# Optimization experiments

Measured on AMD Instinct MI355X. Metric: run time of the kernel, lower is better.

Reference implementation:

```python
import jax, jax.numpy as jnp
import numpy as np

CLIP_LEN = 16
IN_CH = 64  # math.ceil(256 // 4 / 4) * 4
BN_EPS = 1e-5


def setup_inputs() -> dict:
    key = jax.random.key(0)
    ks = jax.random.split(key, 7)
    x = jax.random.normal(ks[0], (128, 256, 56, 56), jnp.float32)
    bn_gamma = 1.0 + 0.1 * jax.random.normal(ks[1], (IN_CH,), jnp.float32)
    bn_beta = 0.1 * jax.random.normal(ks[2], (IN_CH,), jnp.float32)
    bn_mean = 0.1 * jax.random.normal(ks[3], (IN_CH,), jnp.float32)
    bn_var = jax.random.uniform(ks[4], (IN_CH,), jnp.float32, minval=0.5, maxval=1.5)
    # groups=2 Conv3d: out=2, in_per_group=IN_CH//2, kernel 3x3x3
    conv_w = 0.02 * jax.random.normal(ks[5], (2, IN_CH // 2, 3, 3, 3), jnp.float32)
    conv_b = 0.02 * jax.random.normal(ks[6], (2,), jnp.float32)
    return dict(x=x, bn_gamma=bn_gamma, bn_beta=bn_beta, bn_mean=bn_mean,
                bn_var=bn_var, conv_w=conv_w, conv_b=conv_b)


def _gsm(x5, bn_gamma, bn_beta, bn_mean, bn_var, conv_w, conv_b):
    # x5: [n, c, t, h, w] with c == IN_CH
    n, c, t, h, w = x5.shape
    scale = bn_gamma * jax.lax.rsqrt(bn_var + BN_EPS)          # [c]
    shift = bn_beta - bn_mean * scale                          # [c]
    x_act = jax.nn.relu(x5 * scale[None, :, None, None, None]
                        + shift[None, :, None, None, None])
    gate = jnp.tanh(
        jax.lax.conv_general_dilated(
            x_act, conv_w, window_strides=(1, 1, 1), padding='SAME',
            dimension_numbers=('NCDHW', 'OIDHW', 'NCDHW'),
            feature_group_count=2)
        + conv_b[None, :, None, None, None])                   # [n,2,t,h,w]
    half = c // 2

    def gated_shift(xg, g, left):
        y = g * xg                                             # gated part
        r = xg - y                                             # residual part
        if left:
            y_sh = jnp.concatenate([y[:, :, 1:], jnp.zeros_like(y[:, :, :1])], axis=2)
        else:
            y_sh = jnp.concatenate([jnp.zeros_like(y[:, :, :1]), y[:, :, :-1]], axis=2)
        out = y_sh + r
        # channel regroup: [n,2,c/4,t,h,w] -> permute -> [n,c/2,t,h,w]
        return out.reshape(n, 2, half // 2, t, h, w).transpose(0, 2, 1, 3, 4, 5).reshape(n, half, t, h, w)

    y1 = gated_shift(x5[:, :half], gate[:, 0:1], left=True)
    y2 = gated_shift(x5[:, half:], gate[:, 1:2], left=False)
    return jnp.concatenate([y1, y2], axis=1)


def reference(x, bn_gamma, bn_beta, bn_mean, bn_var, conv_w, conv_b):
    nt, c, h, w = x.shape
    n = nt // CLIP_LEN
    # [nt, IN_CH, h, w] -> [n, IN_CH, T, h, w]
    xs = x[:, :IN_CH].reshape(n, CLIP_LEN, IN_CH, h, w).transpose(0, 2, 1, 3, 4)
    y = _gsm(xs, bn_gamma, bn_beta, bn_mean, bn_var, conv_w, conv_b)
    y = y.transpose(0, 2, 1, 3, 4).reshape(nt, IN_CH, h, w)
    # remaining channels pass through unchanged; net wrapper is identity
    return jnp.concatenate([y, x[:, IN_CH:]], axis=1)
```

## Files before the change

kernel.cpp:

```cpp
#include <hip/hip_runtime.h>
#include <hip/hip_cooperative_groups.h>
#include <math.h>

namespace cg = cooperative_groups;

namespace {
constexpr int kT = 16;
constexpr int kH = 56;
constexpr int kW = 56;
constexpr int kCAll = 256;
constexpr int kPlane = kH * kW;
constexpr int kPlane4 = kPlane / 4;
constexpr size_t kGateBytes = (size_t)256 * kPlane * sizeof(float);
constexpr int kSpan = 192 * kPlane4;
constexpr int kFrame4 = kCAll * kPlane4;
}


__device__ __forceinline__ void conv_block(
    int bid, int tid, const float* __restrict__ x,
    const float* __restrict__ gamma, const float* __restrict__ beta,
    const float* __restrict__ mean, const float* __restrict__ var,
    const float* __restrict__ cw, const float* __restrict__ cb,
    float* __restrict__ gate, float4* smb) {
  const int stripe = bid & 1;
  const int g = (bid >> 1) & 1;
  const int t = (bid >> 2) & 15;
  const int n = bid >> 6;
  const int h0 = stripe * 28;
  const int wid = tid >> 6;
  const int lane = tid & 63;
  const int r = lane >> 1;
  const int h = lane & 1;
  const int wbase = wid * 510;

  for (int i = lane; i < 510; i += 64)
    smb[wbase + i] = make_float4(0.f, 0.f, 0.f, 0.f);

  int rr_u[7], fb_u[7], go_u[7];
  bool val_u[7];
  #pragma unroll
  for (int u = 0; u < 7; ++u) {
    const int j = lane + u * 64;
    bool v = (j < 420);
    int rr = 0, fb = 0, go = 0;
    if (v) {
      rr = j / 14;
      fb = j - rr * 14;
      const int gr = h0 + rr - 1;
      v = ((unsigned)gr < (unsigned)kH);
      if (v) go = gr * 14 + fb;
    }
    rr_u[u] = rr; fb_u[u] = fb; go_u[u] = go; val_u[u] = v;
  }

  float acc[28];
  #pragma unroll
  for (int p = 0; p < 28; ++p) acc[p] = 0.f;

  auto loadS = [&](int s, float4 (&pf)[7]) {
    const int il = s / 3;
    const int kd = s - il * 3;
    const int tt = t + kd - 1;
    const int ch = g * 32 + wid * 8 + il;
    if (tt >= 0 && tt < kT) {
      const float4* src4 =
          (const float4*)x + ((size_t)(n * kT + tt) * kCAll + ch) * kPlane4;
      #pragma unroll
      for (int u = 0; u < 7; ++u)
        pf[u] = val_u[u] ? src4[go_u[u]] : make_float4(0.f, 0.f, 0.f, 0.f);
    } else {
      #pragma unroll
      for (int u = 0; u < 7; ++u) pf[u] = make_float4(0.f, 0.f, 0.f, 0.f);
    }
  };

  auto stageS = [&](int s, const float4 (&pf)[7]) {
    const int il = s / 3;
    const int kd = s - il * 3;
    const int tt = t + kd - 1;
    if (tt < 0 || tt >= kT) return;
    const int ch = g * 32 + wid * 8 + il;
    const float sc = gamma[ch] * rsqrtf(var[ch] + 1e-5f);
    const float sh = beta[ch] - mean[ch] * sc;
    #pragma unroll
    for (int u = 0; u < 7; ++u) {
      if (val_u[u]) {
        float4 a = pf[u];
        a.x = fmaxf(0.f, fmaf(a.x, sc, sh));
        a.y = fmaxf(0.f, fmaf(a.y, sc, sh));
        a.z = fmaxf(0.f, fmaf(a.z, sc, sh));
        a.w = fmaxf(0.f, fmaf(a.w, sc, sh));
        smb[wbase + rr_u[u] * 17 + fb_u[u] + 1] = a;
      }
    }
  };

  auto computeS = [&](int s) {
    const int il = s / 3;
    const int kd = s - il * 3;
    const int tt = t + kd - 1;
    if (tt < 0 || tt >= kT) return;
    if (r >= 28) return;
    const int ch = g * 32 + wid * 8 + il;
    const float* wbp = cw + ch * 27 + kd * 9;
    float wk[9];
    #pragma unroll
    for (int j = 0; j < 9; ++j) wk[j] = wbp[j];
    #pragma unroll
    for (int kh = 0; kh < 3; ++kh) {
      const int base = wbase + (r + kh) * 17 + 7 * h;
      float f[36];
      #pragma unroll
      for (int jj = 0; jj < 9; ++jj) {
        const float4 B = smb[base + jj];
        f[4 * jj + 0] = B.x; f[4 * jj + 1] = B.y;
        f[4 * jj + 2] = B.z; f[4 * jj + 3] = B.w;
      }
      const float w0 = wk[kh * 3 + 0];
      const float w1 = wk[kh * 3 + 1];
      const float w2 = wk[kh * 3 + 2];
      #pragma unroll
      for (int p = 0; p < 28; ++p)
        acc[p] = fmaf(f[p + 3], w0,
                 fmaf(f[p + 4], w1, fmaf(f[p + 5], w2, acc[p])));
    }
  };

  float4 A[7], B[7];
  loadS(0, A);
  for (int s2 = 0; s2 < 24; s2 += 2) {
    if (s2 + 1 < 24) loadS(s2 + 1, B);
    stageS(s2, A);
    computeS(s2);
    if (s2 + 2 < 24) loadS(s2 + 2, A);
    if (s2 + 1 < 24) { stageS(s2 + 1, B); computeS(s2 + 1); }
  }

  __syncthreads();
  float* smf = (float*)smb;
  if (r < 28) {
    const int q0 = r * 56 + h * 28;
    #pragma unroll
    for (int p = 0; p < 28; ++p) smf[wid * 1568 + q0 + p] = acc[p];
  }
  __syncthreads();
  const float bias = cb[g];
  float* gp = gate + ((size_t)(n * 2 + g) * kT + t) * kPlane + h0 * kW;
  for (int q = tid; q < 1568; q += 256) {
    float s = smf[q] + smf[1568 + q] + smf[2 * 1568 + q] + smf[3 * 1568 + q];
    gp[q] = tanhf(s + bias);
  }
}

__device__ __forceinline__ void copy_engine(
    int engine, int nengines, int tid, const float4* __restrict__ x4,
    float4* __restrict__ o4, int nf, int skip_hole) {
  const size_t stride = (size_t)nengines * 256;
  const size_t total = (size_t)nf * kSpan;
  size_t j = (size_t)engine * 256 + tid;
  auto mapidx = [&](size_t jj, size_t& idx, bool& ok) {
    const int f = (int)(jj / kSpan);
    const int within = (int)(jj - (size_t)f * kSpan);
    ok = !(skip_hole && f == 126 && within < 3 * kPlane4);
    idx = (size_t)f * kFrame4 + 64 * kPlane4 + within;
  };
  for (; j + 3 * stride < total; j += 4 * stride) {
    size_t i0, i1, i2, i3; bool k0, k1, k2, k3;
    mapidx(j, i0, k0); mapidx(j + stride, i1, k1);
    mapidx(j + 2 * stride, i2, k2); mapidx(j + 3 * stride, i3, k3);
    const float4 a = x4[i0], b = x4[i1], c = x4[i2], d = x4[i3];
    if (k0) o4[i0] = a;
    if (k1) o4[i1] = b;
    if (k2) o4[i2] = c;
    if (k3) o4[i3] = d;
  }
  for (; j < total; j += stride) {
    size_t i0; bool k0;
    mapidx(j, i0, k0);
    const float4 a = x4[i0];
    if (k0) o4[i0] = a;
  }
}

__device__ __forceinline__ void shift_columns(
    int q0, int qstride, const float4* __restrict__ x4,
    const float4* __restrict__ g4, float4* __restrict__ o4) {
  const size_t xstep = (size_t)kFrame4;
  for (int q = q0; q < 8 * 2 * 32 * kPlane4; q += qstride) {
    const int p = q % kPlane4;
    const int rem = q / kPlane4;
    const int m = rem & 31;
    const int half = (rem >> 5) & 1;
    const int n = rem >> 6;
    const int src_ch = half * 32 + m;
    const int k = 2 * (m & 15) + (m >> 4);
    const int c = half * 32 + k;
    const float4* xp = x4 + ((size_t)(n * kT) * kCAll + src_ch) * kPlane4 + p;
    const float4* gp = g4 + (size_t)((n * 2 + half) * kT) * kPlane4 + p;
    float4* op = o4 + ((size_t)(n * kT) * kCAll + c) * kPlane4 + p;
    if (half == 0) {
      float4 xc = xp[0], gc = gp[0];
      #pragma unroll
      for (int t = 0; t < kT; ++t) {
        float4 xn = make_float4(0.f, 0.f, 0.f, 0.f);
        float4 gn = make_float4(0.f, 0.f, 0.f, 0.f);
        if (t < kT - 1) { xn = xp[(size_t)(t + 1) * xstep]; gn = gp[(t + 1) * kPlane4]; }
        float4 res;
        res.x = gn.x * xn.x + xc.x - gc.x * xc.x;
        res.y = gn.y * xn.y + xc.y - gc.y * xc.y;
        res.z = gn.z * xn.z + xc.z - gc.z * xc.z;
        res.w = gn.w * xn.w + xc.w - gc.w * xc.w;
        op[(size_t)t * xstep] = res;
        xc = xn; gc = gn;
      }
    } else {
      float4 xprev = make_float4(0.f, 0.f, 0.f, 0.f);
      float4 gprev = make_float4(0.f, 0.f, 0.f, 0.f);
      #pragma unroll
      for (int t = 0; t < kT; ++t) {
        const float4 xc = xp[(size_t)t * xstep];
        const float4 gc = gp[t * kPlane4];
        float4 res;
        res.x = gprev.x * xprev.x + xc.x - gc.x * xc.x;
        res.y = gprev.y * xprev.y + xc.y - gc.y * xc.y;
        res.z = gprev.z * xprev.z + xc.z - gc.z * xc.z;
        res.w = gprev.w * xprev.w + xc.w - gc.w * xc.w;
        op[(size_t)t * xstep] = res;
        xprev = xc; gprev = gc;
      }
    }
  }
}

__global__ __launch_bounds__(256, 4)
void coop_fused_kernel(const float* __restrict__ x,
                       const float* __restrict__ gamma,
                       const float* __restrict__ beta,
                       const float* __restrict__ mean,
                       const float* __restrict__ var,
                       const float* __restrict__ cw,
                       const float* __restrict__ cb,
                       float* __restrict__ gate,
                       const float4* __restrict__ x4,
                       float4* __restrict__ o4) {
  __shared__ float4 smb[4 * 510];
  if (blockIdx.x & 1)
    conv_block(blockIdx.x >> 1, threadIdx.x, x, gamma, beta, mean, var, cw, cb,
               gate, smb);
  else
    copy_engine(blockIdx.x >> 1, 512, threadIdx.x, x4, o4, 128, 0);
  cg::this_grid().sync();
  shift_columns(blockIdx.x * 256 + threadIdx.x, 1024 * 256, x4,
                (const float4*)gate, o4);
}

__global__ __launch_bounds__(256, 2)
void fused_conv_copy_kernel(const float* __restrict__ x,
                            const float* __restrict__ gamma,
                            const float* __restrict__ beta,
                            const float* __restrict__ mean,
                            const float* __restrict__ var,
                            const float* __restrict__ cw,
                            const float* __restrict__ cb,
                            float* __restrict__ gate,
                            const float4* __restrict__ x4,
                            float4* __restrict__ o4,
                            int nf_copy, int skip_hole) {
  __shared__ float4 smb[4 * 510];
  if ((blockIdx.x & 1) == 0) {
    copy_engine(blockIdx.x >> 1, 512, threadIdx.x, x4, o4, nf_copy, skip_hole);
    return;
  }
  conv_block(blockIdx.x >> 1, threadIdx.x, x, gamma, beta, mean, var, cw, cb,
             gate, smb);
}

__global__ __launch_bounds__(256)
void copy_gate_slice_kernel(float4* __restrict__ o4) {
  const int j = blockIdx.x * 256 + threadIdx.x;
  if (j >= 3 * kPlane4) return;
  const int q = j / kPlane4;
  const int rr = j - q * kPlane4;
  const int pidx = (q == 0) ? 239 : (q == 1 ? 254 : 255);
  const size_t G1 = (size_t)127 * kCAll * kPlane4;
  const size_t H = ((size_t)126 * kCAll + 64) * kPlane4;
  o4[H + j] = o4[G1 + (size_t)pidx * kPlane4 + rr];
}

__global__ __launch_bounds__(256)
void shift_c64_kernel(const float4* __restrict__ x4,
                      const float4* __restrict__ g4,
                      float4* __restrict__ o4, int nf) {
  const size_t total = (size_t)nf * 64 * kPlane4;
  const size_t j = (size_t)blockIdx.x * 256 + threadIdx.x;
  if (j >= total) return;
  const int p = (int)(j % kPlane4);
  const size_t rest = j / kPlane4;
  const int c = (int)(rest % 64);
  const int f = (int)(rest / 64);
  const int n = f >> 4;
  const int t = f & 15;
  const int half = c >> 5;
  const int k = c & 31;
  const int m = ((k & 1) << 4) + (k >> 1);
  const int src_ch = half * 32 + m;
  const size_t xcur = ((size_t)f * kCAll + src_ch) * kPlane4 + p;
  const size_t gbase = (size_t)(n * 2 + half) * kT * kPlane4 + p;
  const float4 xc = x4[xcur];
  const float4 gc = g4[gbase + (size_t)t * kPlane4];
  float4 y = make_float4(0.f, 0.f, 0.f, 0.f);
  if (half == 0) {
    if (t < kT - 1) {
      const float4 xn = x4[xcur + (size_t)kCAll * kPlane4];
      const float4 gn = g4[gbase + (size_t)(t + 1) * kPlane4];
      y.x = gn.x * xn.x; y.y = gn.y * xn.y; y.z = gn.z * xn.z; y.w = gn.w * xn.w;
    }
  } else {
    if (t > 0) {
      const float4 xp = x4[xcur - (size_t)kCAll * kPlane4];
      const float4 gp = g4[gbase + (size_t)(t - 1) * kPlane4];
      y.x = gp.x * xp.x; y.y = gp.y * xp.y; y.z = gp.z * xp.z; y.w = gp.w * xp.w;
    }
  }
  const size_t oidx = ((size_t)f * kCAll + c) * kPlane4 + p;
  float4 res;
  res.x = y.x + (xc.x - gc.x * xc.x);
  res.y = y.y + (xc.y - gc.y * xc.y);
  res.z = y.z + (xc.z - gc.z * xc.z);
  res.w = y.w + (xc.w - gc.w * xc.w);
  o4[oidx] = res;
}

__global__ __launch_bounds__(256)
void last_frame_kernel(const float4* __restrict__ x4, float4* o4) {
  const int idx = blockIdx.x * 256 + threadIdx.x;
  if (idx >= kCAll * kPlane4) return;
  const size_t F127 = (size_t)127 * kCAll * kPlane4;
  const int p = idx % kPlane4;
  const int c = idx / kPlane4;
  if (c >= 64) { o4[F127 + idx] = x4[F127 + idx]; return; }
  const size_t H = ((size_t)126 * kCAll + 64) * kPlane4;
  const int half = c >> 5;
  const int k = c & 31;
  const int m = ((k & 1) << 4) + (k >> 1);
  const int src_ch = half * 32 + m;
  const float4 xc = x4[F127 + (size_t)src_ch * kPlane4 + p];
  float4 gc;
  float4 y = make_float4(0.f, 0.f, 0.f, 0.f);
  if (half == 0) {
    gc = o4[H + 0 * kPlane4 + p];
  } else {
    gc = o4[H + 2 * kPlane4 + p];
    const float4 gp = o4[H + 1 * kPlane4 + p];
    const float4 xp = x4[((size_t)126 * kCAll + src_ch) * kPlane4 + p];
    y.x = gp.x * xp.x; y.y = gp.y * xp.y; y.z = gp.z * xp.z; y.w = gp.w * xp.w;
  }
  float4 res;
  res.x = y.x + (xc.x - gc.x * xc.x);
  res.y = y.y + (xc.y - gc.y * xc.y);
  res.z = y.z + (xc.z - gc.z * xc.z);
  res.w = y.w + (xc.w - gc.w * xc.w);
  o4[F127 + idx] = res;
}

__global__ __launch_bounds__(256)
void fix_hole_kernel(const float4* __restrict__ x4, float4* __restrict__ o4) {
  const int j = blockIdx.x * 256 + threadIdx.x;
  if (j >= 3 * kPlane4) return;
  const size_t H = ((size_t)126 * kCAll + 64) * kPlane4;
  o4[H + j] = x4[H + j];
}

extern "C" void kernel_launch(void* const* d_in, const int* in_sizes, int n_in,
                              void* d_out, int out_size, void* d_ws, size_t ws_size,
                              hipStream_t stream) {
  const float* x     = (const float*)d_in[0];
  const float* gamma = (const float*)d_in[1];
  const float* beta  = (const float*)d_in[2];
  const float* mean  = (const float*)d_in[3];
  const float* var   = (const float*)d_in[4];
  const float* cw    = (const float*)d_in[5];
  const float* cb    = (const float*)d_in[6];
  float* out = (float*)d_out;
  const float4* x4v = (const float4*)x;
  float4* o4v = (float4*)out;

  const bool have_ws = (d_ws != nullptr) && (ws_size >= kGateBytes);

  if (have_ws) {
    int maxBlocks = 0;
    hipError_t qe = hipOccupancyMaxActiveBlocksPerMultiprocessor(
        &maxBlocks, (const void*)coop_fused_kernel, 256, 0);
    if (qe == hipSuccess && maxBlocks >= 4) {
      float* gate = (float*)d_ws;
      void* args[] = {(void*)&x, (void*)&gamma, (void*)&beta, (void*)&mean,
                      (void*)&var, (void*)&cw, (void*)&cb, (void*)&gate,
                      (void*)&x4v, (void*)&o4v};
      hipError_t le = hipLaunchCooperativeKernel(
          (const void*)coop_fused_kernel, dim3(1024), dim3(256), args, 0, stream);
      if (le == hipSuccess) return;
    }
  }

  float* gate = have_ws ? (float*)d_ws : out + (size_t)127 * kCAll * kPlane;
  const int nf = have_ws ? 128 : 127;
  const int skip_hole = have_ws ? 0 : 1;

  fused_conv_copy_kernel<<<1024, 256, 0, stream>>>(
      x, gamma, beta, mean, var, cw, cb, gate, x4v, o4v, nf, skip_hole);

  if (!have_ws)
    copy_gate_slice_kernel<<<10, 256, 0, stream>>>(o4v);

  const int shift_total = nf * 64 * kPlane4;
  shift_c64_kernel<<<(shift_total + 255) / 256, 256, 0, stream>>>(
      x4v, (const float4*)gate, o4v, nf);

  if (!have_ws) {
    last_frame_kernel<<<(kCAll * kPlane4 + 255) / 256, 256, 0, stream>>>(x4v, o4v);
    fix_hole_kernel<<<10, 256, 0, stream>>>(x4v, o4v);
  }
}
```

Baseline: 216.5 us.

## Replace cooperative grid-sync kernel with two ordinary launches for conv/copy and shift

Removes the cooperative kernel that ran conv+copy, then a grid-wide sync, then the shift phase. Instead a normal conv/copy kernel is launched, followed by a separate one-thread-per-column shift kernel (1568 blocks, each thread walking the 16 frames). This drops the grid barrier and the occupancy cap (launch_bounds 256,4 with a fixed 1024-block grid), and gives the shift phase more parallel threads. It adds one extra kernel launch and relies on stream ordering for the dependency.

```diff
diff --git a/kernel.cpp b/kernel.cpp
--- a/kernel.cpp
+++ b/kernel.cpp
@@ -1,8 +1,5 @@
 #include <hip/hip_runtime.h>
-#include <hip/hip_cooperative_groups.h>
 #include <math.h>
-
-namespace cg = cooperative_groups;
 
 namespace {
 constexpr int kT = 16;
@@ -183,78 +180,6 @@
   }
 }
 
-__device__ __forceinline__ void shift_columns(
-    int q0, int qstride, const float4* __restrict__ x4,
-    const float4* __restrict__ g4, float4* __restrict__ o4) {
-  const size_t xstep = (size_t)kFrame4;
-  for (int q = q0; q < 8 * 2 * 32 * kPlane4; q += qstride) {
-    const int p = q % kPlane4;
-    const int rem = q / kPlane4;
-    const int m = rem & 31;
-    const int half = (rem >> 5) & 1;
-    const int n = rem >> 6;
-    const int src_ch = half * 32 + m;
-    const int k = 2 * (m & 15) + (m >> 4);
-    const int c = half * 32 + k;
-    const float4* xp = x4 + ((size_t)(n * kT) * kCAll + src_ch) * kPlane4 + p;
-    const float4* gp = g4 + (size_t)((n * 2 + half) * kT) * kPlane4 + p;
-    float4* op = o4 + ((size_t)(n * kT) * kCAll + c) * kPlane4 + p;
-    if (half == 0) {
-      float4 xc = xp[0], gc = gp[0];
-      #pragma unroll
-      for (int t = 0; t < kT; ++t) {
-        float4 xn = make_float4(0.f, 0.f, 0.f, 0.f);
-        float4 gn = make_float4(0.f, 0.f, 0.f, 0.f);
-        if (t < kT - 1) { xn = xp[(size_t)(t + 1) * xstep]; gn = gp[(t + 1) * kPlane4]; }
-        float4 res;
-        res.x = gn.x * xn.x + xc.x - gc.x * xc.x;
-        res.y = gn.y * xn.y + xc.y - gc.y * xc.y;
-        res.z = gn.z * xn.z + xc.z - gc.z * xc.z;
-        res.w = gn.w * xn.w + xc.w - gc.w * xc.w;
-        op[(size_t)t * xstep] = res;
-        xc = xn; gc = gn;
-      }
-    } else {
-      float4 xprev = make_float4(0.f, 0.f, 0.f, 0.f);
-      float4 gprev = make_float4(0.f, 0.f, 0.f, 0.f);
-      #pragma unroll
-      for (int t = 0; t < kT; ++t) {
-        const float4 xc = xp[(size_t)t * xstep];
-        const float4 gc = gp[t * kPlane4];
-        float4 res;
-        res.x = gprev.x * xprev.x + xc.x - gc.x * xc.x;
-        res.y = gprev.y * xprev.y + xc.y - gc.y * xc.y;
-        res.z = gprev.z * xprev.z + xc.z - gc.z * xc.z;
-        res.w = gprev.w * xprev.w + xc.w - gc.w * xc.w;
-        op[(size_t)t * xstep] = res;
-        xprev = xc; gprev = gc;
-      }
-    }
-  }
-}
-
-__global__ __launch_bounds__(256, 4)
-void coop_fused_kernel(const float* __restrict__ x,
-                       const float* __restrict__ gamma,
-                       const float* __restrict__ beta,
-                       const float* __restrict__ mean,
-                       const float* __restrict__ var,
-                       const float* __restrict__ cw,
-                       const float* __restrict__ cb,
-                       float* __restrict__ gate,
-                       const float4* __restrict__ x4,
-                       float4* __restrict__ o4) {
-  __shared__ float4 smb[4 * 510];
-  if (blockIdx.x & 1)
-    conv_block(blockIdx.x >> 1, threadIdx.x, x, gamma, beta, mean, var, cw, cb,
-               gate, smb);
-  else
-    copy_engine(blockIdx.x >> 1, 512, threadIdx.x, x4, o4, 128, 0);
-  cg::this_grid().sync();
-  shift_columns(blockIdx.x * 256 + threadIdx.x, 1024 * 256, x4,
-                (const float4*)gate, o4);
-}
-
 __global__ __launch_bounds__(256, 2)
 void fused_conv_copy_kernel(const float* __restrict__ x,
                             const float* __restrict__ gamma,
@@ -274,6 +199,56 @@
   }
   conv_block(blockIdx.x >> 1, threadIdx.x, x, gamma, beta, mean, var, cw, cb,
              gate, smb);
+}
+
+__global__ __launch_bounds__(256)
+void shift_columns_kernel(const float4* __restrict__ x4,
+                          const float4* __restrict__ g4,
+                          float4* __restrict__ o4) {
+  const int q = blockIdx.x * 256 + threadIdx.x;
+  const size_t xstep = (size_t)kFrame4;
+  const int p = q % kPlane4;
+  const int rem = q / kPlane4;
+  const int m = rem & 31;
+  const int half = (rem >> 5) & 1;
+  const int n = rem >> 6;
+  const int src_ch = half * 32 + m;
+  const int k = 2 * (m & 15) + (m >> 4);
+  const int c = half * 32 + k;
+  const float4* xp = x4 + ((size_t)(n * kT) * kCAll + src_ch) * kPlane4 + p;
+  const float4* gp = g4 + (size_t)((n * 2 + half) * kT) * kPlane4 + p;
+  float4* op = o4 + ((size_t)(n * kT) * kCAll + c) * kPlane4 + p;
+  if (half == 0) {
+    float4 xc = xp[0], gc = gp[0];
+    #pragma unroll
+    for (int t = 0; t < kT; ++t) {
+      float4 xn = make_float4(0.f, 0.f, 0.f, 0.f);
+      float4 gn = make_float4(0.f, 0.f, 0.f, 0.f);
+      if (t < kT - 1) { xn = xp[(size_t)(t + 1) * xstep]; gn = gp[(t + 1) * kPlane4]; }
+      float4 res;
+      res.x = gn.x * xn.x + xc.x - gc.x * xc.x;
+      res.y = gn.y * xn.y + xc.y - gc.y * xc.y;
+      res.z = gn.z * xn.z + xc.z - gc.z * xc.z;
+      res.w = gn.w * xn.w + xc.w - gc.w * xc.w;
+      op[(size_t)t * xstep] = res;
+      xc = xn; gc = gn;
+    }
+  } else {
+    float4 xprev = make_float4(0.f, 0.f, 0.f, 0.f);
+    float4 gprev = make_float4(0.f, 0.f, 0.f, 0.f);
+    #pragma unroll
+    for (int t = 0; t < kT; ++t) {
+      const float4 xc = xp[(size_t)t * xstep];
+      const float4 gc = gp[t * kPlane4];
+      float4 res;
+      res.x = gprev.x * xprev.x + xc.x - gc.x * xc.x;
+      res.y = gprev.y * xprev.y + xc.y - gc.y * xc.y;
+      res.z = gprev.z * xprev.z + xc.z - gc.z * xc.z;
+      res.w = gprev.w * xprev.w + xc.w - gc.w * xc.w;
+      op[(size_t)t * xstep] = res;
+      xprev = xc; gprev = gc;
+    }
+  }
 }
 
 __global__ __launch_bounds__(256)
@@ -387,22 +362,6 @@
   float4* o4v = (float4*)out;
 
   const bool have_ws = (d_ws != nullptr) && (ws_size >= kGateBytes);
-
-  if (have_ws) {
-    int maxBlocks = 0;
-    hipError_t qe = hipOccupancyMaxActiveBlocksPerMultiprocessor(
-        &maxBlocks, (const void*)coop_fused_kernel, 256, 0);
-    if (qe == hipSuccess && maxBlocks >= 4) {
-      float* gate = (float*)d_ws;
-      void* args[] = {(void*)&x, (void*)&gamma, (void*)&beta, (void*)&mean,
-                      (void*)&var, (void*)&cw, (void*)&cb, (void*)&gate,
-                      (void*)&x4v, (void*)&o4v};
-      hipError_t le = hipLaunchCooperativeKernel(
-          (const void*)coop_fused_kernel, dim3(1024), dim3(256), args, 0, stream);
-      if (le == hipSuccess) return;
-    }
-  }
-
   float* gate = have_ws ? (float*)d_ws : out + (size_t)127 * kCAll * kPlane;
   const int nf = have_ws ? 128 : 127;
   const int skip_hole = have_ws ? 0 : 1;
@@ -410,14 +369,14 @@
   fused_conv_copy_kernel<<<1024, 256, 0, stream>>>(
       x, gamma, beta, mean, var, cw, cb, gate, x4v, o4v, nf, skip_hole);
 
-  if (!have_ws)
+  if (have_ws) {
+    shift_columns_kernel<<<1568, 256, 0, stream>>>(
+        x4v, (const float4*)gate, o4v);
+  } else {
     copy_gate_slice_kernel<<<10, 256, 0, stream>>>(o4v);
-
-  const int shift_total = nf * 64 * kPlane4;
-  shift_c64_kernel<<<(shift_total + 255) / 256, 256, 0, stream>>>(
-      x4v, (const float4*)gate, o4v, nf);
-
-  if (!have_ws) {
+    const int shift_total = nf * 64 * kPlane4;
+    shift_c64_kernel<<<(shift_total + 255) / 256, 256, 0, stream>>>(
+        x4v, (const float4*)gate, o4v, nf);
     last_frame_kernel<<<(kCAll * kPlane4 + 255) / 256, 256, 0, stream>>>(x4v, o4v);
     fix_hole_kernel<<<10, 256, 0, stream>>>(x4v, o4v);
   }
```

Result: faster. 210.3 us (-2.8%).
